# Kernel optimization log

Hardware: AMD Instinct MI355X
Metric: run time of the kernel (lower is better)

Reference implementation:

```python
import jax, jax.numpy as jnp
import numpy as np


def setup_inputs() -> dict:
    key = jax.random.key(0)
    ks = jax.random.split(key, 6)
    B, N_IN, N_OUT, C_IN, C_OUT, S, NNZ = 16, 6250, 25000, 64, 64, 9, 75000
    x = jax.random.normal(ks[0], (B, N_IN, C_IN), dtype=jnp.float32)
    trans_values = jax.random.uniform(ks[1], (NNZ,), dtype=jnp.float32)
    trans_row = jax.random.randint(ks[2], (NNZ,), 0, N_OUT, dtype=jnp.int32)
    trans_col = jax.random.randint(ks[3], (NNZ,), 0, N_IN, dtype=jnp.int32)
    spiral_indices = jax.random.randint(ks[4], (N_OUT, S), 0, N_OUT, dtype=jnp.int32)
    # Linear(S*C_IN -> C_OUT), kaiming-ish scale
    W = jax.random.normal(ks[5], (S * C_IN, C_OUT), dtype=jnp.float32) * (1.0 / np.sqrt(S * C_IN))
    b = jnp.zeros((C_OUT,), dtype=jnp.float32)
    return {"x": x, "trans_values": trans_values, "trans_row": trans_row,
            "trans_col": trans_col, "spiral_indices": spiral_indices,
            "W": W, "b": b, "n_out": N_OUT}


def reference(x, trans_values, trans_row, trans_col, spiral_indices, W, b, n_out):
    B, N_in, C = x.shape
    # Pool: gather cols, scale by sparse values, scatter-add to rows
    gathered = x[:, trans_col, :] * trans_values[None, :, None]        # [B, nnz, C]
    pooled = jnp.zeros((B, n_out, C), x.dtype).at[:, trans_row].add(gathered)  # [B, n_out, C]
    # SpiralConv: gather spiral neighborhoods, flatten, linear
    S = spiral_indices.shape[1]
    feat = pooled[:, spiral_indices, :].reshape(B, n_out, S * C)       # [B, n_out, S*C]
    out = feat @ W + b                                                 # [B, n_out, C_out]
    return jax.nn.elu(out)
```

## Files before the change

kernel.cpp:

```cpp
#include <hip/hip_runtime.h>

#define B_     16
#define N_IN_  6250
#define N_OUT_ 25000
#define C_     64
#define S_     9
#define NNZ_   75000
#define PROW_  (B_ * C_)

typedef __bf16 bf16x8 __attribute__((ext_vector_type(8)));
typedef float floatx4 __attribute__((ext_vector_type(4)));


__global__ void hist_kernel(const int* __restrict__ rows, int* __restrict__ counts, int nnz) {
    int i = blockIdx.x * blockDim.x + threadIdx.x;
    if (i < nnz) atomicAdd(&counts[rows[i]], 1);
}

__global__ void scan1_kernel(const int* __restrict__ counts, int* __restrict__ offsets,
                             int* __restrict__ bsum, int n) {
    __shared__ int wsum[16];
    int t = threadIdx.x;
    int wid = t >> 6, lane = t & 63;
    int i = blockIdx.x * 1024 + t;
    int v = (i < n) ? counts[i] : 0;
    int s = v;
    #pragma unroll
    for (int d = 1; d < 64; d <<= 1) {
        int u = __shfl_up(s, d, 64);
        if (lane >= d) s += u;
    }
    if (lane == 63) wsum[wid] = s;
    __syncthreads();
    if (wid == 0 && lane < 16) {
        int ws = wsum[lane];
        #pragma unroll
        for (int d = 1; d < 16; d <<= 1) {
            int u = __shfl_up(ws, d, 64);
            if (lane >= d) ws += u;
        }
        wsum[lane] = ws;
    }
    __syncthreads();
    int wave_off = (wid == 0) ? 0 : wsum[wid - 1];
    int incl = s + wave_off;
    if (i < n) offsets[i] = incl - v;
    if (t == 1023) bsum[blockIdx.x] = incl;
}

__global__ void scan2_kernel(int* __restrict__ bsum, int* __restrict__ offsets, int nblk, int n) {
    if (threadIdx.x == 0) {
        int t = 0;
        for (int i = 0; i < nblk; ++i) { int v = bsum[i]; bsum[i] = t; t += v; }
        offsets[n] = t;
    }
}

__global__ void scan3_kernel(int* __restrict__ offsets, const int* __restrict__ bsum,
                             int* __restrict__ cursor, int n) {
    int i = blockIdx.x * 1024 + threadIdx.x;
    if (i < n) {
        int o = offsets[i] + bsum[blockIdx.x];
        offsets[i] = o;
        cursor[i] = o;
    }
}

__global__ void fill_kernel(const int* __restrict__ rows, const int* __restrict__ cols,
                            const float* __restrict__ vals, int* __restrict__ cursor,
                            int* __restrict__ ecol, float* __restrict__ eval, int nnz) {
    int i = blockIdx.x * blockDim.x + threadIdx.x;
    if (i < nnz) {
        int p = atomicAdd(&cursor[rows[i]], 1);
        ecol[p] = cols[i];
        eval[p] = vals[i];
    }
}

__global__ __launch_bounds__(256) void pool_kernel(
        const float* __restrict__ x, const int* __restrict__ offsets,
        const int* __restrict__ ecol, const float* __restrict__ eval,
        __bf16* __restrict__ pooled) {
    __shared__ int   scol[64];
    __shared__ float sval[64];
    int row = blockIdx.x;
    int t = threadIdx.x;
    int c = t & 63, bq = t >> 6;
    int beg = offsets[row], end = offsets[row + 1];
    int count = end - beg;

    float acc[4] = {0.f, 0.f, 0.f, 0.f};
    for (int base = 0; base < count; base += 64) {
        int nb = min(64, count - base);
        if (t < nb) {
            scol[t] = ecol[beg + base + t];
            sval[t] = eval[beg + base + t];
        }
        __syncthreads();
        for (int k = 0; k < nb; ++k) {
            int col = scol[k];
            float v = sval[k];
            const float* xp = x + ((size_t)col * C_ + c);
            #pragma unroll
            for (int j = 0; j < 4; ++j) {
                acc[j] += xp[(size_t)(bq * 4 + j) * N_IN_ * C_] * v;
            }
        }
        __syncthreads();
    }
    #pragma unroll
    for (int j = 0; j < 4; ++j) {
        pooled[(size_t)row * PROW_ + (bq * 4 + j) * C_ + c] = (__bf16)acc[j];
    }
}

__global__ void convw_kernel(const float* __restrict__ W, __bf16* __restrict__ Wt) {
    int i = blockIdx.x * blockDim.x + threadIdx.x;
    if (i < 576 * 64) {
        int k = i >> 6, n = i & 63;
        Wt[n * 576 + k] = (__bf16)W[i];
    }
}

__global__ __launch_bounds__(256, 2) void gemm_kernel(
        const __bf16* __restrict__ pooled, const int* __restrict__ spiral,
        const __bf16* __restrict__ Wt, const float* __restrict__ bias,
        float* __restrict__ out) {
    int b0 = blockIdx.y * 4;
    int t = threadIdx.x;
    int wave = t >> 6, lane = t & 63;
    int quad = lane >> 4, l16 = lane & 15;
    int mbase = blockIdx.x * 64 + wave * 16;
    int m = mbase + l16;
    int mc = (m < N_OUT_) ? m : 0;

    int src[S_];
    #pragma unroll
    for (int s = 0; s < S_; ++s) src[s] = spiral[mc * S_ + s];

    floatx4 acc[4][4] = {};
    bf16x8 aA[8], aB[8], bA[8], bB[8];

    auto aload = [&](int s, bf16x8* a) {
        const __bf16* base = pooled + (size_t)src[s] * PROW_ + quad * 8;
        #pragma unroll
        for (int j = 0; j < 4; ++j)
            #pragma unroll
            for (int kc = 0; kc < 2; ++kc)
                a[j * 2 + kc] = *reinterpret_cast<const bf16x8*>(
                    base + (b0 + j) * C_ + kc * 32);
    };
    auto bload = [&](int s, bf16x8* bb) {
        const __bf16* base = Wt + l16 * 576 + s * 64 + quad * 8;
        #pragma unroll
        for (int nt = 0; nt < 4; ++nt)
            #pragma unroll
            for (int kc = 0; kc < 2; ++kc)
                bb[nt * 2 + kc] = *reinterpret_cast<const bf16x8*>(
                    base + nt * 16 * 576 + kc * 32);
    };
    auto mmac = [&](bf16x8* a, bf16x8* bb) {
        #pragma unroll
        for (int kc = 0; kc < 2; ++kc)
            #pragma unroll
            for (int j = 0; j < 4; ++j)
                #pragma unroll
                for (int nt = 0; nt < 4; ++nt)
                    acc[j][nt] = __builtin_amdgcn_mfma_f32_16x16x32_bf16(
                        a[j * 2 + kc], bb[nt * 2 + kc], acc[j][nt], 0, 0, 0);
    };

    aload(0, aA); bload(0, bA);
    #pragma unroll
    for (int sp = 0; sp < 4; ++sp) {
        int s = sp * 2;
        aload(s + 1, aB); bload(s + 1, bB);
        mmac(aA, bA);
        aload(s + 2, aA); bload(s + 2, bA);
        mmac(aB, bB);
    }
    mmac(aA, bA);

    #pragma unroll
    for (int nt = 0; nt < 4; ++nt) {
        float bn = bias[nt * 16 + l16];
        #pragma unroll
        for (int j = 0; j < 4; ++j) {
            #pragma unroll
            for (int i = 0; i < 4; ++i) {
                int mm = mbase + quad * 4 + i;
                if (mm < N_OUT_) {
                    float v = acc[j][nt][i] + bn;
                    v = (v > 0.0f) ? v : expm1f(v);
                    out[((size_t)(b0 + j) * N_OUT_ + mm) * C_ + nt * 16 + l16] = v;
                }
            }
        }
    }
}

extern "C" void kernel_launch(void* const* d_in, const int* in_sizes, int n_in,
                              void* d_out, int out_size, void* d_ws, size_t ws_size,
                              hipStream_t stream) {
    const float* x      = (const float*)d_in[0];
    const float* tvals  = (const float*)d_in[1];
    const int*   trow   = (const int*)d_in[2];
    const int*   tcol   = (const int*)d_in[3];
    const int*   spiral = (const int*)d_in[4];
    const float* W      = (const float*)d_in[5];
    const float* bias   = (const float*)d_in[6];
    float* out = (float*)d_out;

    char* ws = (char*)d_ws;
    size_t off = 0;
    auto alloc = [&](size_t bytes) -> void* {
        void* p = ws + off;
        off += (bytes + 255) & ~(size_t)255;
        return p;
    };
    __bf16* pooled  = (__bf16*)alloc((size_t)N_OUT_ * PROW_ * 2);
    __bf16* Wt      = (__bf16*)alloc(576 * 64 * 2);
    int*    cursor  = (int*)alloc(N_OUT_ * 4);
    int*    offsets = (int*)alloc((N_OUT_ + 1) * 4);
    int*    ecol    = (int*)alloc(NNZ_ * 4);
    float*  eval    = (float*)alloc(NNZ_ * 4);
    int*    counts  = (int*)alloc(N_OUT_ * 4);
    int*    bsum    = (int*)alloc(32 * 4);

    const int NBLK = (N_OUT_ + 1023) / 1024;
    hipMemsetAsync(counts, 0, N_OUT_ * 4, stream);
    hist_kernel<<<(NNZ_ + 255) / 256, 256, 0, stream>>>(trow, counts, NNZ_);
    scan1_kernel<<<NBLK, 1024, 0, stream>>>(counts, offsets, bsum, N_OUT_);
    scan2_kernel<<<1, 64, 0, stream>>>(bsum, offsets, NBLK, N_OUT_);
    scan3_kernel<<<NBLK, 1024, 0, stream>>>(offsets, bsum, cursor, N_OUT_);
    fill_kernel<<<(NNZ_ + 255) / 256, 256, 0, stream>>>(trow, tcol, tvals, cursor, ecol, eval, NNZ_);
    pool_kernel<<<N_OUT_, 256, 0, stream>>>(x, offsets, ecol, eval, pooled);
    convw_kernel<<<(576 * 64 + 255) / 256, 256, 0, stream>>>(W, Wt);
    gemm_kernel<<<dim3((N_OUT_ + 63) / 64, 4), 256, 0, stream>>>(pooled, spiral, Wt, bias, out);
}
```

Measured before the change: 326.2 us.

## Relayout pooled per batch and map batches to XCDs for L2 locality

Pooled storage moves from row-major [n_out][B*C] to batch-major [B][n_out][C]. Both the pool and GEMM kernels now swizzle block indices so each XCD (blockIdx & 7) handles one or two fixed batches, which keeps that batch's x and pooled slices resident in its L2. The GEMM now gives each wave 16 output channels over 64 rows, keeps all W fragments in registers, and triple-buffers the gathered A loads, all aimed at cutting redundant global traffic. In exchange each gathered row is only 128 bytes, so memory accesses are less coalesced, and the design assumes round-robin dispatch of blocks across XCDs.

Result: slower. 549.1 us (+68.4%).

```diff
diff --git a/kernel.cpp b/kernel.cpp
--- a/kernel.cpp
+++ b/kernel.cpp
@@ -6,7 +6,7 @@
 #define C_     64
 #define S_     9
 #define NNZ_   75000
-#define PROW_  (B_ * C_)
+#define MT_    391
 
 typedef __bf16 bf16x8 __attribute__((ext_vector_type(8)));
 typedef float floatx4 __attribute__((ext_vector_type(4)));
@@ -81,37 +81,25 @@
         const float* __restrict__ x, const int* __restrict__ offsets,
         const int* __restrict__ ecol, const float* __restrict__ eval,
         __bf16* __restrict__ pooled) {
-    __shared__ int   scol[64];
-    __shared__ float sval[64];
-    int row = blockIdx.x;
+    int bx = blockIdx.x;
+    int xcd = bx & 7;
+    int rr = bx >> 3;
+    int half = (rr >= 6250) ? 1 : 0;
+    int rq = rr - half * 6250;
+    int b = xcd + 8 * half;
     int t = threadIdx.x;
-    int c = t & 63, bq = t >> 6;
+    int row = rq * 4 + (t >> 6);
+    int c = t & 63;
+
     int beg = offsets[row], end = offsets[row + 1];
-    int count = end - beg;
-
-    float acc[4] = {0.f, 0.f, 0.f, 0.f};
-    for (int base = 0; base < count; base += 64) {
-        int nb = min(64, count - base);
-        if (t < nb) {
-            scol[t] = ecol[beg + base + t];
-            sval[t] = eval[beg + base + t];
-        }
-        __syncthreads();
-        for (int k = 0; k < nb; ++k) {
-            int col = scol[k];
-            float v = sval[k];
-            const float* xp = x + ((size_t)col * C_ + c);
-            #pragma unroll
-            for (int j = 0; j < 4; ++j) {
-                acc[j] += xp[(size_t)(bq * 4 + j) * N_IN_ * C_] * v;
-            }
-        }
-        __syncthreads();
-    }
-    #pragma unroll
-    for (int j = 0; j < 4; ++j) {
-        pooled[(size_t)row * PROW_ + (bq * 4 + j) * C_ + c] = (__bf16)acc[j];
-    }
+    const float* xb = x + (size_t)b * N_IN_ * C_;
+    float acc = 0.0f;
+    for (int k = beg; k < end; ++k) {
+        int col = ecol[k];
+        float v = eval[k];
+        acc += xb[(size_t)col * C_ + c] * v;
+    }
+    pooled[((size_t)b * N_OUT_ + row) * C_ + c] = (__bf16)acc;
 }
 
 __global__ void convw_kernel(const float* __restrict__ W, __bf16* __restrict__ Wt) {
@@ -126,74 +114,81 @@
         const __bf16* __restrict__ pooled, const int* __restrict__ spiral,
         const __bf16* __restrict__ Wt, const float* __restrict__ bias,
         float* __restrict__ out) {
-    int b0 = blockIdx.y * 4;
+    int bx = blockIdx.x;
+    int xcd = bx & 7;
+    int rr = bx >> 3;
+    int half = (rr >= MT_) ? 1 : 0;
+    int mt = rr - half * MT_;
+    int b = xcd + 8 * half;
+
     int t = threadIdx.x;
     int wave = t >> 6, lane = t & 63;
     int quad = lane >> 4, l16 = lane & 15;
-    int mbase = blockIdx.x * 64 + wave * 16;
-    int m = mbase + l16;
-    int mc = (m < N_OUT_) ? m : 0;
-
-    int src[S_];
-    #pragma unroll
-    for (int s = 0; s < S_; ++s) src[s] = spiral[mc * S_ + s];
-
-    floatx4 acc[4][4] = {};
-    bf16x8 aA[8], aB[8], bA[8], bB[8];
-
-    auto aload = [&](int s, bf16x8* a) {
-        const __bf16* base = pooled + (size_t)src[s] * PROW_ + quad * 8;
-        #pragma unroll
-        for (int j = 0; j < 4; ++j)
+    int mbase = mt * 64;
+
+    const __bf16* poolb = pooled + (size_t)b * N_OUT_ * C_;
+
+    int src[4][S_];
+    #pragma unroll
+    for (int mi = 0; mi < 4; ++mi) {
+        int m = mbase + mi * 16 + l16;
+        int mc = (m < N_OUT_) ? m : 0;
+        #pragma unroll
+        for (int s = 0; s < S_; ++s) src[mi][s] = spiral[mc * S_ + s];
+    }
+
+    bf16x8 Bf[S_][2];
+    {
+        const __bf16* wbase = Wt + (wave * 16 + l16) * 576 + quad * 8;
+        #pragma unroll
+        for (int s = 0; s < S_; ++s)
             #pragma unroll
             for (int kc = 0; kc < 2; ++kc)
-                a[j * 2 + kc] = *reinterpret_cast<const bf16x8*>(
-                    base + (b0 + j) * C_ + kc * 32);
-    };
-    auto bload = [&](int s, bf16x8* bb) {
-        const __bf16* base = Wt + l16 * 576 + s * 64 + quad * 8;
-        #pragma unroll
-        for (int nt = 0; nt < 4; ++nt)
+                Bf[s][kc] = *reinterpret_cast<const bf16x8*>(wbase + s * 64 + kc * 32);
+    }
+
+    floatx4 acc[4] = {};
+    bf16x8 Ab[3][4][2];
+
+    auto aload = [&](int s, bf16x8 (*buf)[2]) {
+        #pragma unroll
+        for (int mi = 0; mi < 4; ++mi)
             #pragma unroll
             for (int kc = 0; kc < 2; ++kc)
-                bb[nt * 2 + kc] = *reinterpret_cast<const bf16x8*>(
-                    base + nt * 16 * 576 + kc * 32);
+                buf[mi][kc] = *reinterpret_cast<const bf16x8*>(
+                    poolb + (size_t)src[mi][s] * C_ + kc * 32 + quad * 8);
     };
-    auto mmac = [&](bf16x8* a, bf16x8* bb) {
-        #pragma unroll
-        for (int kc = 0; kc < 2; ++kc)
-            #pragma unroll
-            for (int j = 0; j < 4; ++j)
-                #pragma unroll
-                for (int nt = 0; nt < 4; ++nt)
-                    acc[j][nt] = __builtin_amdgcn_mfma_f32_16x16x32_bf16(
-                        a[j * 2 + kc], bb[nt * 2 + kc], acc[j][nt], 0, 0, 0);
-    };
-
-    aload(0, aA); bload(0, bA);
-    #pragma unroll
-    for (int sp = 0; sp < 4; ++sp) {
-        int s = sp * 2;
-        aload(s + 1, aB); bload(s + 1, bB);
-        mmac(aA, bA);
-        aload(s + 2, aA); bload(s + 2, bA);
-        mmac(aB, bB);
-    }
-    mmac(aA, bA);
-
-    #pragma unroll
-    for (int nt = 0; nt < 4; ++nt) {
-        float bn = bias[nt * 16 + l16];
-        #pragma unroll
-        for (int j = 0; j < 4; ++j) {
-            #pragma unroll
-            for (int i = 0; i < 4; ++i) {
-                int mm = mbase + quad * 4 + i;
-                if (mm < N_OUT_) {
-                    float v = acc[j][nt][i] + bn;
-                    v = (v > 0.0f) ? v : expm1f(v);
-                    out[((size_t)(b0 + j) * N_OUT_ + mm) * C_ + nt * 16 + l16] = v;
-                }
+
+    aload(0, Ab[0]);
+    aload(1, Ab[1]);
+    aload(2, Ab[2]);
+    __builtin_amdgcn_sched_barrier(0);
+
+    #pragma unroll
+    for (int s = 0; s < S_; ++s) {
+        bf16x8 (*cur)[2] = Ab[s % 3];
+        #pragma unroll
+        for (int mi = 0; mi < 4; ++mi) {
+            acc[mi] = __builtin_amdgcn_mfma_f32_16x16x32_bf16(cur[mi][0], Bf[s][0], acc[mi], 0, 0, 0);
+            acc[mi] = __builtin_amdgcn_mfma_f32_16x16x32_bf16(cur[mi][1], Bf[s][1], acc[mi], 0, 0, 0);
+        }
+        if (s + 3 < S_) {
+            aload(s + 3, Ab[s % 3]);
+            __builtin_amdgcn_sched_barrier(0);
+        }
+    }
+
+    float bn = bias[wave * 16 + l16];
+    float* outb = out + (size_t)b * N_OUT_ * C_;
+    #pragma unroll
+    for (int mi = 0; mi < 4; ++mi) {
+        #pragma unroll
+        for (int i = 0; i < 4; ++i) {
+            int m = mbase + mi * 16 + quad * 4 + i;
+            if (m < N_OUT_) {
+                float v = acc[mi][i] + bn;
+                v = (v > 0.0f) ? v : expm1f(v);
+                outb[(size_t)m * C_ + wave * 16 + l16] = v;
             }
         }
     }
@@ -218,7 +213,7 @@
         off += (bytes + 255) & ~(size_t)255;
         return p;
     };
-    __bf16* pooled  = (__bf16*)alloc((size_t)N_OUT_ * PROW_ * 2);
+    __bf16* pooled  = (__bf16*)alloc((size_t)B_ * N_OUT_ * C_ * 2);
     __bf16* Wt      = (__bf16*)alloc(576 * 64 * 2);
     int*    cursor  = (int*)alloc(N_OUT_ * 4);
     int*    offsets = (int*)alloc((N_OUT_ + 1) * 4);
@@ -234,7 +229,7 @@
     scan2_kernel<<<1, 64, 0, stream>>>(bsum, offsets, NBLK, N_OUT_);
     scan3_kernel<<<NBLK, 1024, 0, stream>>>(offsets, bsum, cursor, N_OUT_);
     fill_kernel<<<(NNZ_ + 255) / 256, 256, 0, stream>>>(trow, tcol, tvals, cursor, ecol, eval, NNZ_);
-    pool_kernel<<<N_OUT_, 256, 0, stream>>>(x, offsets, ecol, eval, pooled);
+    pool_kernel<<<8 * 12500, 256, 0, stream>>>(x, offsets, ecol, eval, pooled);
     convw_kernel<<<(576 * 64 + 255) / 256, 256, 0, stream>>>(W, Wt);
-    gemm_kernel<<<dim3((N_OUT_ + 63) / 64, 4), 256, 0, stream>>>(pooled, spiral, Wt, bias, out);
-}
+    gemm_kernel<<<8 * (2 * MT_), 256, 0, stream>>>(pooled, spiral, Wt, bias, out);
+}
```

## Store pooled batch-major, stage W in LDS, one batch per block with XCD mapping

Applied to the files above, without the earlier changes.

Pooled features move from a row-major [row][batch][channel] layout to batch-major [batch][row][channel]. Each GEMM block now handles a single batch and 64 output rows. The full transposed weight matrix is copied into padded LDS with async global-to-LDS loads instead of being re-read from global memory per spiral step. Block indices are arranged so each XCD handles a fixed batch, aiming for better L2 locality on the gathered pooled rows. The trade-off is four times more blocks that each reload all of W into LDS, which adds about 75KB of LDS per block and lowers occupancy.

Measured after the change: 300.0 us. 8.0% less time.

```diff
diff --git a/kernel.cpp b/kernel.cpp
--- a/kernel.cpp
+++ b/kernel.cpp
@@ -6,10 +6,17 @@
 #define C_     64
 #define S_     9
 #define NNZ_   75000
-#define PROW_  (B_ * C_)
+#define MT_    391
+#define BROW_  584
 
 typedef __bf16 bf16x8 __attribute__((ext_vector_type(8)));
 typedef float floatx4 __attribute__((ext_vector_type(4)));
+
+__device__ inline void async_copy16(const void* g, void* l) {
+    __builtin_amdgcn_global_load_lds(
+        (const __attribute__((address_space(1))) void*)g,
+        (__attribute__((address_space(3))) void*)l, 16, 0, 0);
+}
 
 
 __global__ void hist_kernel(const int* __restrict__ rows, int* __restrict__ counts, int nnz) {
@@ -110,7 +117,7 @@
     }
     #pragma unroll
     for (int j = 0; j < 4; ++j) {
-        pooled[(size_t)row * PROW_ + (bq * 4 + j) * C_ + c] = (__bf16)acc[j];
+        pooled[((size_t)(bq * 4 + j) * N_OUT_ + row) * C_ + c] = (__bf16)acc[j];
     }
 }
 
@@ -126,74 +133,76 @@
         const __bf16* __restrict__ pooled, const int* __restrict__ spiral,
         const __bf16* __restrict__ Wt, const float* __restrict__ bias,
         float* __restrict__ out) {
-    int b0 = blockIdx.y * 4;
+    __shared__ __bf16 Bs[64 * BROW_];
+
+    int bx = blockIdx.x;
+    int xcd = bx & 7;
+    int rr = bx >> 3;
+    int half = (rr >= MT_) ? 1 : 0;
+    int mt = rr - half * MT_;
+    int b = xcd + 8 * half;
+
     int t = threadIdx.x;
     int wave = t >> 6, lane = t & 63;
     int quad = lane >> 4, l16 = lane & 15;
-    int mbase = blockIdx.x * 64 + wave * 16;
+    int mbase = mt * 64 + wave * 16;
     int m = mbase + l16;
     int mc = (m < N_OUT_) ? m : 0;
 
+    for (int j = t; j < (64 * BROW_ * 2) / 16; j += 256) {
+        int col = j / 73;
+        int rem = j - col * 73;
+        async_copy16((const char*)Wt + col * 1152 + rem * 16,
+                     (char*)Bs + j * 16);
+    }
+
     int src[S_];
     #pragma unroll
     for (int s = 0; s < S_; ++s) src[s] = spiral[mc * S_ + s];
 
-    floatx4 acc[4][4] = {};
-    bf16x8 aA[8], aB[8], bA[8], bB[8];
-
-    auto aload = [&](int s, bf16x8* a) {
-        const __bf16* base = pooled + (size_t)src[s] * PROW_ + quad * 8;
+    const __bf16* poolb = pooled + (size_t)b * N_OUT_ * C_;
+
+    __syncthreads();
+
+    floatx4 acc[4] = {};
+    bf16x8 Acur[2], Anxt[2];
+
+    auto loadA = [&](int s, bf16x8* A) {
+        const __bf16* p = poolb + (size_t)src[s] * C_ + quad * 8;
+        A[0] = *reinterpret_cast<const bf16x8*>(p);
+        A[1] = *reinterpret_cast<const bf16x8*>(p + 32);
+    };
+
+    loadA(0, Acur);
+    #pragma unroll
+    for (int s = 0; s < S_; ++s) {
+        if (s + 1 < S_) {
+            loadA(s + 1, (s & 1) ? Acur : Anxt);
+            __builtin_amdgcn_sched_barrier(0);
+        }
+        bf16x8* A = (s & 1) ? Anxt : Acur;
         #pragma unroll
-        for (int j = 0; j < 4; ++j)
+        for (int kc = 0; kc < 2; ++kc) {
             #pragma unroll
-            for (int kc = 0; kc < 2; ++kc)
-                a[j * 2 + kc] = *reinterpret_cast<const bf16x8*>(
-                    base + (b0 + j) * C_ + kc * 32);
-    };
-    auto bload = [&](int s, bf16x8* bb) {
-        const __bf16* base = Wt + l16 * 576 + s * 64 + quad * 8;
-        #pragma unroll
-        for (int nt = 0; nt < 4; ++nt)
-            #pragma unroll
-            for (int kc = 0; kc < 2; ++kc)
-                bb[nt * 2 + kc] = *reinterpret_cast<const bf16x8*>(
-                    base + nt * 16 * 576 + kc * 32);
-    };
-    auto mmac = [&](bf16x8* a, bf16x8* bb) {
-        #pragma unroll
-        for (int kc = 0; kc < 2; ++kc)
-            #pragma unroll
-            for (int j = 0; j < 4; ++j)
-                #pragma unroll
-                for (int nt = 0; nt < 4; ++nt)
-                    acc[j][nt] = __builtin_amdgcn_mfma_f32_16x16x32_bf16(
-                        a[j * 2 + kc], bb[nt * 2 + kc], acc[j][nt], 0, 0, 0);
-    };
-
-    aload(0, aA); bload(0, bA);
-    #pragma unroll
-    for (int sp = 0; sp < 4; ++sp) {
-        int s = sp * 2;
-        aload(s + 1, aB); bload(s + 1, bB);
-        mmac(aA, bA);
-        aload(s + 2, aA); bload(s + 2, bA);
-        mmac(aB, bB);
-    }
-    mmac(aA, bA);
-
+            for (int nt = 0; nt < 4; ++nt) {
+                bf16x8 bb = *reinterpret_cast<const bf16x8*>(
+                    &Bs[(nt * 16 + l16) * BROW_ + s * 64 + kc * 32 + quad * 8]);
+                acc[nt] = __builtin_amdgcn_mfma_f32_16x16x32_bf16(A[kc], bb, acc[nt], 0, 0, 0);
+            }
+        }
+    }
+
+    float* outb = out + (size_t)b * N_OUT_ * C_;
     #pragma unroll
     for (int nt = 0; nt < 4; ++nt) {
         float bn = bias[nt * 16 + l16];
         #pragma unroll
-        for (int j = 0; j < 4; ++j) {
-            #pragma unroll
-            for (int i = 0; i < 4; ++i) {
-                int mm = mbase + quad * 4 + i;
-                if (mm < N_OUT_) {
-                    float v = acc[j][nt][i] + bn;
-                    v = (v > 0.0f) ? v : expm1f(v);
-                    out[((size_t)(b0 + j) * N_OUT_ + mm) * C_ + nt * 16 + l16] = v;
-                }
+        for (int i = 0; i < 4; ++i) {
+            int mm = mbase + quad * 4 + i;
+            if (mm < N_OUT_) {
+                float v = acc[nt][i] + bn;
+                v = (v > 0.0f) ? v : expm1f(v);
+                outb[(size_t)mm * C_ + nt * 16 + l16] = v;
             }
         }
     }
@@ -218,7 +227,7 @@
         off += (bytes + 255) & ~(size_t)255;
         return p;
     };
-    __bf16* pooled  = (__bf16*)alloc((size_t)N_OUT_ * PROW_ * 2);
+    __bf16* pooled  = (__bf16*)alloc((size_t)B_ * N_OUT_ * C_ * 2);
     __bf16* Wt      = (__bf16*)alloc(576 * 64 * 2);
     int*    cursor  = (int*)alloc(N_OUT_ * 4);
     int*    offsets = (int*)alloc((N_OUT_ + 1) * 4);
@@ -236,5 +245,5 @@
     fill_kernel<<<(NNZ_ + 255) / 256, 256, 0, stream>>>(trow, tcol, tvals, cursor, ecol, eval, NNZ_);
     pool_kernel<<<N_OUT_, 256, 0, stream>>>(x, offsets, ecol, eval, pooled);
     convw_kernel<<<(576 * 64 + 255) / 256, 256, 0, stream>>>(W, Wt);
-    gemm_kernel<<<dim3((N_OUT_ + 63) / 64, 4), 256, 0, stream>>>(pooled, spiral, Wt, bias, out);
-}
+    gemm_kernel<<<8 * (2 * MT_), 256, 0, stream>>>(pooled, spiral, Wt, bias, out);
+}
```
